# Optimization experiments

Measured on AMD Instinct MI355X. Metric: run time of the kernel, lower is better.

## Reference

```python
import jax, jax.numpy as jnp
import numpy as np

MAX_LORAS, OUT, IN = 8, 4096, 4096
B, S = 4, 2048


def setup_inputs() -> dict:
    key = jax.random.key(0)
    k1, k2, k3 = jax.random.split(key, 3)
    x = jax.random.normal(k1, (B, S, IN), dtype=jnp.float32)
    weight = jax.random.normal(k2, (MAX_LORAS, OUT, IN), dtype=jnp.float32) * 0.02
    adapter_ids = jax.random.randint(k3, (B,), 0, MAX_LORAS, dtype=jnp.int32)
    return {"x": x, "weight": weight, "adapter_ids": adapter_ids}


def reference(x, weight, adapter_ids):
    # Gather a full [OUT, IN] matrix per batch element (matches weight[adapter_ids]).
    w = weight[adapter_ids]                 # [B, OUT, IN]
    # F.linear(x, w) == x @ w^T, batched over B: [B, S, IN] x [B, OUT, IN] -> [B, S, OUT]
    return jnp.einsum('bsi,boi->bso', x, w)
```

## Files before the change

### kernel.cpp

```cpp
#include <hip/hip_runtime.h>
#include <hip/hip_bf16.h>


#define SEQ    2048
#define IN_K   4096
#define OUT_N  4096
#define NB     4

typedef __attribute__((ext_vector_type(8))) short  short8;
typedef __attribute__((ext_vector_type(4))) float  float4v;

constexpr int BM = 256, BN = 256, BK = 32;
constexpr int GT = 512;
constexpr int KTILES = IN_K / BK;

__device__ inline short f2b(float f) {
    union { float f; unsigned u; } v; v.f = f;
    unsigned r = v.u + 0x7FFFu + ((v.u >> 16) & 1u);
    return (short)(r >> 16);
}
__device__ inline short8 pack8(float4v lo, float4v hi) {
    short8 r;
    r[0] = f2b(lo[0]); r[1] = f2b(lo[1]); r[2] = f2b(lo[2]); r[3] = f2b(lo[3]);
    r[4] = f2b(hi[0]); r[5] = f2b(hi[1]); r[6] = f2b(hi[2]); r[7] = f2b(hi[3]);
    return r;
}

typedef const __attribute__((address_space(1))) void* gp1_t;
typedef __attribute__((address_space(3))) void*       lp3_t;
__device__ inline void gload_lds16(const void* g, void* l) {
    __builtin_amdgcn_global_load_lds((gp1_t)g, (lp3_t)l, 16, 0, 0);
}

#define WAITV(N)  asm volatile("s_waitcnt vmcnt(" #N ")" ::: "memory")
#define WAITL0()  asm volatile("s_waitcnt lgkmcnt(0)" ::: "memory")

__global__ __launch_bounds__(256)
void cvt_x_kernel(const float* __restrict__ x, short* __restrict__ o, int n8)
{
    int i = blockIdx.x * blockDim.x + threadIdx.x;
    const int stride = gridDim.x * blockDim.x;
    for (; i < n8; i += stride) {
        const float4v a = *(const float4v*)(x + (size_t)i * 8);
        const float4v b = *(const float4v*)(x + (size_t)i * 8 + 4);
        *(short8*)(o + (size_t)i * 8) = pack8(a, b);
    }
}

__global__ __launch_bounds__(256)
void cvt_w_kernel(const float* __restrict__ w, const int* __restrict__ ids,
                  short* __restrict__ o)
{
    const int b = blockIdx.y;
    const float* __restrict__ src = w + (size_t)ids[b] * OUT_N * IN_K;
    short* __restrict__ dst = o + (size_t)b * OUT_N * IN_K;
    const int n8 = OUT_N * IN_K / 8;
    int i = blockIdx.x * blockDim.x + threadIdx.x;
    const int stride = gridDim.x * blockDim.x;
    for (; i < n8; i += stride) {
        const float4v a = *(const float4v*)(src + (size_t)i * 8);
        const float4v c = *(const float4v*)(src + (size_t)i * 8 + 4);
        *(short8*)(dst + (size_t)i * 8) = pack8(a, c);
    }
}

__global__ __launch_bounds__(GT, 2)
void mll_gemm_8ph(const short* __restrict__ A, const short* __restrict__ W4,
                  float* __restrict__ out)
{
    __shared__ __align__(16) short lds[4][2 * BM * BK];

    const int tid  = threadIdx.x;
    const int lane = tid & 63;
    const int wid  = tid >> 6;
    const int wr   = wid >> 2;
    const int wc   = wid & 3;

    const int bid = blockIdx.x;
    const int n   = (bid & 7) * 64 + (bid >> 3);
    const int bx  = n & 15;
    const int by  = (n >> 4) & 7;
    const int bz  = n >> 7;
    const int brow = by * BM, bcol = bx * BN;

    const short* __restrict__ Ab = A  + (size_t)bz * SEQ   * IN_K + (size_t)brow * IN_K;
    const short* __restrict__ Bb = W4 + (size_t)bz * OUT_N * IN_K + (size_t)bcol * IN_K;

    const int c0 = tid, c1 = tid + GT;
    const short* pa0 = Ab + (size_t)(c0 >> 2) * IN_K + (c0 & 3) * 8;
    const short* pa1 = Ab + (size_t)(c1 >> 2) * IN_K + (c1 & 3) * 8;
    const short* pb0 = Bb + (size_t)(c0 >> 2) * IN_K + (c0 & 3) * 8;
    const short* pb1 = Bb + (size_t)(c1 >> 2) * IN_K + (c1 & 3) * 8;

    float4v acc[8][4];
#pragma unroll
    for (int m = 0; m < 8; ++m)
#pragma unroll
        for (int q = 0; q < 4; ++q)
            acc[m][q] = (float4v){0.f, 0.f, 0.f, 0.f};

    const int lr  = lane & 15;
    const int ksl = lane >> 4;

#pragma unroll
    for (int tt = 0; tt < 3; ++tt) {
        short* s = &lds[tt][0];
        gload_lds16(pa0 + tt * BK, s + c0 * 8);
        gload_lds16(pa1 + tt * BK, s + c1 * 8);
        gload_lds16(pb0 + tt * BK, s + BM * BK + c0 * 8);
        gload_lds16(pb1 + tt * BK, s + BM * BK + c1 * 8);
    }

    for (int t = 0; t < KTILES; ++t) {
        if (t <= KTILES - 3)      WAITV(8);
        else if (t == KTILES - 2) WAITV(4);
        else                      WAITV(0);
        __builtin_amdgcn_s_barrier();

        const short* sA = &lds[t & 3][0];
        const short* sB = sA + BM * BK;
        short8 af[4], bf[4];

#pragma unroll
        for (int m = 0; m < 4; ++m)
            af[m] = *(const short8*)(sA + (wr * 128 + m * 16 + lr) * BK + ksl * 8);
#pragma unroll
        for (int q = 0; q < 4; ++q)
            bf[q] = *(const short8*)(sB + (wc * 64 + q * 16 + lr) * BK + ksl * 8);
        if (t <= KTILES - 4) {
            short* d = &lds[(t + 3) & 3][0];
            gload_lds16(pa0 + (t + 3) * BK, d + c0 * 8);
            gload_lds16(pa1 + (t + 3) * BK, d + c1 * 8);
        }
        WAITL0();
        __builtin_amdgcn_s_setprio(1);
#pragma unroll
        for (int m = 0; m < 4; ++m)
#pragma unroll
            for (int q = 0; q < 4; ++q)
                acc[m][q] = __builtin_amdgcn_mfma_f32_16x16x32_bf16(
                    af[m], bf[q], acc[m][q], 0, 0, 0);
        __builtin_amdgcn_s_setprio(0);
        __builtin_amdgcn_s_barrier();

#pragma unroll
        for (int m = 0; m < 4; ++m)
            af[m] = *(const short8*)(sA + (wr * 128 + (m + 4) * 16 + lr) * BK + ksl * 8);
        if (t <= KTILES - 4) {
            short* d = &lds[(t + 3) & 3][0];
            gload_lds16(pb0 + (t + 3) * BK, d + BM * BK + c0 * 8);
            gload_lds16(pb1 + (t + 3) * BK, d + BM * BK + c1 * 8);
        }
        WAITL0();
        __builtin_amdgcn_s_setprio(1);
#pragma unroll
        for (int m = 0; m < 4; ++m)
#pragma unroll
            for (int q = 0; q < 4; ++q)
                acc[m + 4][q] = __builtin_amdgcn_mfma_f32_16x16x32_bf16(
                    af[m], bf[q], acc[m + 4][q], 0, 0, 0);
        __builtin_amdgcn_s_setprio(0);
    }

    float* __restrict__ ob = out + (size_t)bz * SEQ * OUT_N;
    const int lrow = ksl * 4;
#pragma unroll
    for (int m = 0; m < 8; ++m) {
#pragma unroll
        for (int q = 0; q < 4; ++q) {
            const int r0 = brow + wr * 128 + m * 16 + lrow;
            const int c  = bcol + wc * 64 + q * 16 + lr;
#pragma unroll
            for (int j = 0; j < 4; ++j)
                ob[(size_t)(r0 + j) * OUT_N + c] = acc[m][q][j];
        }
    }
}

__device__ inline int xr(int row) { return (row & 3) ^ ((row >> 2) & 3); }

__global__ __launch_bounds__(256, 2)
void mll_gemm_fused(const float* __restrict__ x,
                    const float* __restrict__ w,
                    const int*   __restrict__ adapter_ids,
                    float* __restrict__ out)
{
    constexpr int FBM = 128, FBN = 128, FBK = 32;
    __shared__ __align__(16) short As[2][FBM * FBK];
    __shared__ __align__(16) short Bs[2][FBN * FBK];

    const int tid  = threadIdx.x;
    const int lane = tid & 63;
    const int wave = tid >> 6;
    const int wr   = wave >> 1;
    const int wc   = wave & 1;

    const int b    = blockIdx.z;
    const int aid  = adapter_ids[b];
    const int brow = blockIdx.y * FBM;
    const int bcol = blockIdx.x * FBN;

    const float* __restrict__ xb = x + (size_t)b   * SEQ   * IN_K;
    const float* __restrict__ wb = w + (size_t)aid * OUT_N * IN_K;

    float4v ra[2][2], rb[2][2];

    auto LOADG = [&](int kt) {
        const int k0 = kt * FBK;
#pragma unroll
        for (int g = 0; g < 2; ++g) {
            const int f  = tid + g * 256;
            const int r  = f >> 2;
            const int sl = f & 3;
            const float* pa = xb + (size_t)(brow + r) * IN_K + k0 + sl * 8;
            ra[g][0] = *(const float4v*)pa;
            ra[g][1] = *(const float4v*)(pa + 4);
            const float* pb = wb + (size_t)(bcol + r) * IN_K + k0 + sl * 8;
            rb[g][0] = *(const float4v*)pb;
            rb[g][1] = *(const float4v*)(pb + 4);
        }
    };
    auto STORE_LDS = [&](int buf) {
#pragma unroll
        for (int g = 0; g < 2; ++g) {
            const int f  = tid + g * 256;
            const int r  = f >> 2;
            const int sl = f & 3;
            const int ss = sl ^ xr(r);
            *(short8*)&As[buf][r * FBK + ss * 8] = pack8(ra[g][0], ra[g][1]);
            *(short8*)&Bs[buf][r * FBK + ss * 8] = pack8(rb[g][0], rb[g][1]);
        }
    };

    float4v acc[4][4];
#pragma unroll
    for (int m = 0; m < 4; ++m)
#pragma unroll
        for (int q = 0; q < 4; ++q)
            acc[m][q] = (float4v){0.f, 0.f, 0.f, 0.f};

    const int NT = IN_K / FBK;
    LOADG(0); STORE_LDS(0); __syncthreads();
    int cur = 0;
    for (int kt = 0; kt < NT; ++kt) {
        if (kt + 1 < NT) LOADG(kt + 1);
        short8 af[4], bfr[4];
        const int ksl = lane >> 4;
#pragma unroll
        for (int m = 0; m < 4; ++m) {
            const int rr = wr * 64 + m * 16 + (lane & 15);
            af[m] = *(const short8*)&As[cur][rr * FBK + (ksl ^ xr(rr)) * 8];
        }
#pragma unroll
        for (int q = 0; q < 4; ++q) {
            const int rc = wc * 64 + q * 16 + (lane & 15);
            bfr[q] = *(const short8*)&Bs[cur][rc * FBK + (ksl ^ xr(rc)) * 8];
        }
#pragma unroll
        for (int m = 0; m < 4; ++m)
#pragma unroll
            for (int q = 0; q < 4; ++q)
                acc[m][q] = __builtin_amdgcn_mfma_f32_16x16x32_bf16(
                    af[m], bfr[q], acc[m][q], 0, 0, 0);
        if (kt + 1 < NT) STORE_LDS(cur ^ 1);
        __syncthreads();
        cur ^= 1;
    }

    float* __restrict__ ob = out + (size_t)b * SEQ * OUT_N;
    const int lrow = (lane >> 4) * 4;
    const int lcol = lane & 15;
#pragma unroll
    for (int m = 0; m < 4; ++m) {
#pragma unroll
        for (int q = 0; q < 4; ++q) {
            const int r0 = brow + wr * 64 + m * 16 + lrow;
            const int c  = bcol + wc * 64 + q * 16 + lcol;
#pragma unroll
            for (int j = 0; j < 4; ++j)
                ob[(size_t)(r0 + j) * OUT_N + c] = acc[m][q][j];
        }
    }
}

extern "C" void kernel_launch(void* const* d_in, const int* in_sizes, int n_in,
                              void* d_out, int out_size, void* d_ws, size_t ws_size,
                              hipStream_t stream)
{
    const float* x   = (const float*)d_in[0];
    const float* w   = (const float*)d_in[1];
    const int*   ids = (const int*)d_in[2];
    float* out = (float*)d_out;

    const size_t xb_bytes = (size_t)NB * SEQ   * IN_K * sizeof(short);
    const size_t wb_bytes = (size_t)NB * OUT_N * IN_K * sizeof(short);

    if (ws_size >= xb_bytes + wb_bytes) {
        short* xb16 = (short*)d_ws;
        short* wb16 = (short*)((char*)d_ws + xb_bytes);
        cvt_x_kernel<<<2048, 256, 0, stream>>>(x, xb16, NB * SEQ * IN_K / 8);
        cvt_w_kernel<<<dim3(1024, NB), 256, 0, stream>>>(w, ids, wb16);
        mll_gemm_8ph<<<512, GT, 0, stream>>>(xb16, wb16, out);
    } else {
        mll_gemm_fused<<<dim3(OUT_N / 128, SEQ / 128, NB), 256, 0, stream>>>(
            x, w, ids, out);
    }
}
```

Measured before the change: 370.6 us.

## Software-pipeline LDS fragment loads across phases and dedupe weight conversion by adapter id

The GEMM main loop is restructured so the next tile's A/B fragments are read from LDS right after the current tile's second MFMA phase, and the barrier/vmcnt waits are moved so that LDS reads overlap MFMA work. Separately, weight conversion now writes into a slot indexed by adapter id and skips batch entries whose id repeats, so duplicate adapters are converted only once. The GEMM then looks up the weight slot through ids. This needs a larger workspace (room for 8 adapters) and keeps a fallback path, and it changes the wait counts, which risks hazards if they are miscounted.

```diff
diff --git a/kernel.cpp b/kernel.cpp
--- a/kernel.cpp
+++ b/kernel.cpp
@@ -49,11 +49,17 @@
 
 __global__ __launch_bounds__(256)
 void cvt_w_kernel(const float* __restrict__ w, const int* __restrict__ ids,
-                  short* __restrict__ o)
-{
-    const int b = blockIdx.y;
-    const float* __restrict__ src = w + (size_t)ids[b] * OUT_N * IN_K;
-    short* __restrict__ dst = o + (size_t)b * OUT_N * IN_K;
+                  short* __restrict__ o, int by_id)
+{
+    const int b  = blockIdx.y;
+    const int id = ids[b];
+    int slot = b;
+    if (by_id) {
+        for (int j = 0; j < b; ++j) if (ids[j] == id) return;
+        slot = id;
+    }
+    const float* __restrict__ src = w + (size_t)id   * OUT_N * IN_K;
+    short* __restrict__       dst = o + (size_t)slot * OUT_N * IN_K;
     const int n8 = OUT_N * IN_K / 8;
     int i = blockIdx.x * blockDim.x + threadIdx.x;
     const int stride = gridDim.x * blockDim.x;
@@ -65,8 +71,8 @@
 }
 
 __global__ __launch_bounds__(GT, 2)
-void mll_gemm_8ph(const short* __restrict__ A, const short* __restrict__ W4,
-                  float* __restrict__ out)
+void mll_gemm_v4(const short* __restrict__ A, const short* __restrict__ W,
+                 const int* __restrict__ ids, int by_id, float* __restrict__ out)
 {
     __shared__ __align__(16) short lds[4][2 * BM * BK];
 
@@ -83,8 +89,9 @@
     const int bz  = n >> 7;
     const int brow = by * BM, bcol = bx * BN;
 
-    const short* __restrict__ Ab = A  + (size_t)bz * SEQ   * IN_K + (size_t)brow * IN_K;
-    const short* __restrict__ Bb = W4 + (size_t)bz * OUT_N * IN_K + (size_t)bcol * IN_K;
+    const int wslot = by_id ? ids[bz] : bz;
+    const short* __restrict__ Ab = A + (size_t)bz * SEQ * IN_K + (size_t)brow * IN_K;
+    const short* __restrict__ Bb = W + (size_t)wslot * OUT_N * IN_K + (size_t)bcol * IN_K;
 
     const int c0 = tid, c1 = tid + GT;
     const short* pa0 = Ab + (size_t)(c0 >> 2) * IN_K + (c0 & 3) * 8;
@@ -110,56 +117,71 @@
         gload_lds16(pb0 + tt * BK, s + BM * BK + c0 * 8);
         gload_lds16(pb1 + tt * BK, s + BM * BK + c1 * 8);
     }
-
-    for (int t = 0; t < KTILES; ++t) {
-        if (t <= KTILES - 3)      WAITV(8);
-        else if (t == KTILES - 2) WAITV(4);
-        else                      WAITV(0);
-        __builtin_amdgcn_s_barrier();
-
-        const short* sA = &lds[t & 3][0];
+    WAITV(8);
+    __builtin_amdgcn_s_barrier();
+
+    short8 af_a[4], af_b[4], bf[4];
+    {
+        const short* sA = &lds[0][0];
         const short* sB = sA + BM * BK;
-        short8 af[4], bf[4];
-
-#pragma unroll
-        for (int m = 0; m < 4; ++m)
-            af[m] = *(const short8*)(sA + (wr * 128 + m * 16 + lr) * BK + ksl * 8);
+#pragma unroll
+        for (int m = 0; m < 4; ++m)
+            af_a[m] = *(const short8*)(sA + (wr * 128 + m * 16 + lr) * BK + ksl * 8);
 #pragma unroll
         for (int q = 0; q < 4; ++q)
             bf[q] = *(const short8*)(sB + (wc * 64 + q * 16 + lr) * BK + ksl * 8);
+    }
+
+    for (int t = 0; t < KTILES; ++t) {
+        const short* sA = &lds[t & 3][0];
+
+        WAITL0();
+        __builtin_amdgcn_s_setprio(1);
+#pragma unroll
+        for (int m = 0; m < 4; ++m)
+#pragma unroll
+            for (int q = 0; q < 4; ++q)
+                acc[m][q] = __builtin_amdgcn_mfma_f32_16x16x32_bf16(
+                    af_a[m], bf[q], acc[m][q], 0, 0, 0);
+        __builtin_amdgcn_s_setprio(0);
+#pragma unroll
+        for (int m = 0; m < 4; ++m)
+            af_b[m] = *(const short8*)(sA + (wr * 128 + (m + 4) * 16 + lr) * BK + ksl * 8);
         if (t <= KTILES - 4) {
             short* d = &lds[(t + 3) & 3][0];
             gload_lds16(pa0 + (t + 3) * BK, d + c0 * 8);
             gload_lds16(pa1 + (t + 3) * BK, d + c1 * 8);
         }
+        if (t <= KTILES - 4)      WAITV(6);
+        else if (t == KTILES - 3) WAITV(4);
+        else if (t == KTILES - 2) WAITV(0);
+        __builtin_amdgcn_s_barrier();
+
         WAITL0();
         __builtin_amdgcn_s_setprio(1);
 #pragma unroll
         for (int m = 0; m < 4; ++m)
 #pragma unroll
             for (int q = 0; q < 4; ++q)
-                acc[m][q] = __builtin_amdgcn_mfma_f32_16x16x32_bf16(
-                    af[m], bf[q], acc[m][q], 0, 0, 0);
+                acc[m + 4][q] = __builtin_amdgcn_mfma_f32_16x16x32_bf16(
+                    af_b[m], bf[q], acc[m + 4][q], 0, 0, 0);
         __builtin_amdgcn_s_setprio(0);
-        __builtin_amdgcn_s_barrier();
-
-#pragma unroll
-        for (int m = 0; m < 4; ++m)
-            af[m] = *(const short8*)(sA + (wr * 128 + (m + 4) * 16 + lr) * BK + ksl * 8);
+        if (t < KTILES - 1) {
+            const short* sN = &lds[(t + 1) & 3][0];
+            const short* sNB = sN + BM * BK;
+#pragma unroll
+            for (int m = 0; m < 4; ++m)
+                af_a[m] = *(const short8*)(sN + (wr * 128 + m * 16 + lr) * BK + ksl * 8);
+#pragma unroll
+            for (int q = 0; q < 4; ++q)
+                bf[q] = *(const short8*)(sNB + (wc * 64 + q * 16 + lr) * BK + ksl * 8);
+        }
         if (t <= KTILES - 4) {
             short* d = &lds[(t + 3) & 3][0];
             gload_lds16(pb0 + (t + 3) * BK, d + BM * BK + c0 * 8);
             gload_lds16(pb1 + (t + 3) * BK, d + BM * BK + c1 * 8);
         }
-        WAITL0();
-        __builtin_amdgcn_s_setprio(1);
-#pragma unroll
-        for (int m = 0; m < 4; ++m)
-#pragma unroll
-            for (int q = 0; q < 4; ++q)
-                acc[m + 4][q] = __builtin_amdgcn_mfma_f32_16x16x32_bf16(
-                    af[m], bf[q], acc[m + 4][q], 0, 0, 0);
-        __builtin_amdgcn_s_setprio(0);
+        __builtin_amdgcn_s_barrier();
     }
 
     float* __restrict__ ob = out + (size_t)bz * SEQ * OUT_N;
@@ -292,15 +314,22 @@
     const int*   ids = (const int*)d_in[2];
     float* out = (float*)d_out;
 
-    const size_t xb_bytes = (size_t)NB * SEQ   * IN_K * sizeof(short);
-    const size_t wb_bytes = (size_t)NB * OUT_N * IN_K * sizeof(short);
-
-    if (ws_size >= xb_bytes + wb_bytes) {
+    const size_t xb_bytes   = (size_t)NB * SEQ   * IN_K * sizeof(short);
+    const size_t wb4_bytes  = (size_t)NB * OUT_N * IN_K * sizeof(short);
+    const size_t wb8_bytes  = (size_t)8  * OUT_N * IN_K * sizeof(short);
+
+    if (ws_size >= xb_bytes + wb8_bytes) {
         short* xb16 = (short*)d_ws;
         short* wb16 = (short*)((char*)d_ws + xb_bytes);
         cvt_x_kernel<<<2048, 256, 0, stream>>>(x, xb16, NB * SEQ * IN_K / 8);
-        cvt_w_kernel<<<dim3(1024, NB), 256, 0, stream>>>(w, ids, wb16);
-        mll_gemm_8ph<<<512, GT, 0, stream>>>(xb16, wb16, out);
+        cvt_w_kernel<<<dim3(1024, NB), 256, 0, stream>>>(w, ids, wb16, 1);
+        mll_gemm_v4<<<512, GT, 0, stream>>>(xb16, wb16, ids, 1, out);
+    } else if (ws_size >= xb_bytes + wb4_bytes) {
+        short* xb16 = (short*)d_ws;
+        short* wb16 = (short*)((char*)d_ws + xb_bytes);
+        cvt_x_kernel<<<2048, 256, 0, stream>>>(x, xb16, NB * SEQ * IN_K / 8);
+        cvt_w_kernel<<<dim3(1024, NB), 256, 0, stream>>>(w, ids, wb16, 0);
+        mll_gemm_v4<<<512, GT, 0, stream>>>(xb16, wb16, ids, 0, out);
     } else {
         mll_gemm_fused<<<dim3(OUT_N / 128, SEQ / 128, NB), 256, 0, stream>>>(
             x, w, ids, out);
```

Measured after the change: 339.1 us. -8.5%, faster.
